# Kernel optimization log

Measured on AMD Instinct MI355X. Metric: run time of the kernel, lower is better.

The kernel has to match this reference:

```python
import jax, jax.numpy as jnp
import numpy as np

EPS = 1e-15
PROJ_EPS = 4e-3  # float32 boundary eps (geoopt convention)

def _artanh(x):
    return jnp.arctanh(jnp.clip(x, -1.0 + 1e-7, 1.0 - 1e-7))

def _norm(x, axis=-1):
    return jnp.maximum(jnp.sqrt(jnp.sum(x * x, axis=axis, keepdims=True)), EPS)

def expmap0(u, c):
    sc = jnp.sqrt(c)
    n = _norm(u)
    return jnp.tanh(sc * n) * u / (sc * n)

def project(x, c):
    n = _norm(x)
    maxn = (1.0 - PROJ_EPS) / jnp.sqrt(c)
    return jnp.where(n > maxn, x / n * maxn, x)

def mobius_pointwise_mul(w, x, c):
    sc = jnp.sqrt(c)
    wx = w * x
    xn = _norm(x)
    wxn = _norm(wx)
    return jnp.tanh(wxn / xn * _artanh(sc * xn)) * wx / (wxn * sc)

def mobius_add(x, y, c):
    x2 = jnp.sum(x * x, -1, keepdims=True)
    y2 = jnp.sum(y * y, -1, keepdims=True)
    xy = jnp.sum(x * y, -1, keepdims=True)
    num = (1.0 + 2.0 * c * xy + c * y2) * x + (1.0 - c * x2) * y
    den = 1.0 + 2.0 * c * xy + (c ** 2) * x2 * y2
    return num / jnp.maximum(den, EPS)

def logmap0(y, c):
    sc = jnp.sqrt(c)
    n = _norm(y)
    return _artanh(sc * n) * y / (sc * n)

def weighted_midpoint_batched(mix, c):
    # mix: (B, D, L); feature axis = 1 (torch call: dim=0 per sample), reduce over L.
    lam = 2.0 / jnp.maximum(1.0 - c * jnp.sum(mix * mix, axis=1, keepdims=True), EPS)  # (B,1,L)
    nom = jnp.sum(lam * mix, axis=2)          # (B, D)
    den = jnp.sum(lam - 1.0, axis=2)          # (B, 1)
    den = jnp.where(den >= 0, jnp.maximum(den, 1e-10), jnp.minimum(den, -1e-10))
    tm = nom / den                            # (B, D) "two_mean"
    # mobius_scalar_mul(0.5, tm)
    sc = jnp.sqrt(c)
    n = _norm(tm)
    return jnp.tanh(0.5 * _artanh(sc * n)) * tm / (sc * n)

def setup_inputs() -> dict:
    key = jax.random.key(0)
    ks = jax.random.split(key, 7)
    B, O, L, D = 64, 1, 1024, 1024
    return {
        "query": jax.random.normal(ks[0], (B, O, D), jnp.float32),
        "context": jax.random.normal(ks[1], (B, L, D), jnp.float32),
        "delta_t": jax.random.uniform(ks[2], (B, 1, L), jnp.float32),
        "c": jnp.ones((1,), jnp.float32),
        "W_in": jax.random.normal(ks[3], (D, D), jnp.float32) / np.float32(np.sqrt(D)),
        "W_out": jax.random.normal(ks[4], (D, 2 * D), jnp.float32) / np.float32(np.sqrt(2 * D)),
        "ae": jax.random.normal(ks[5], (B, 1, 1), jnp.float32) * 0.1,
        "ab": jax.random.normal(ks[6], (B, 1, 1), jnp.float32) * 0.1,
    }

def reference(query, context, delta_t, c, W_in, W_out, ae, ab):
    # linear_in (attention_type='general'): no bias
    q = jnp.einsum('bod,ed->boe', query, W_in)                     # (B,O,D)
    scores = jnp.einsum('bod,bld->bol', q, context)                # (B,O,L)
    aw = jax.nn.softmax(scores, axis=-1)
    aw = project(expmap0(aw, c), c)                                # hyperbolic attn weights
    ctx_t = jnp.transpose(context, (0, 2, 1))                      # (B,D,L)
    mix = project(mobius_pointwise_mul(aw, ctx_t, c), c)           # (B,D,L)
    bt = jnp.exp(-ab * delta_t)                                    # (B,1,L)
    bt = project(expmap0(bt, c), c)
    tmp = project(mobius_pointwise_mul(ae, mix, c), c)
    tmp = project(mobius_pointwise_mul(tmp, bt, c), c)
    term2 = jax.nn.relu(tmp)
    mix = project(mobius_add(mix, term2, c), c)
    fin = weighted_midpoint_batched(mix, c)[:, None, :]            # (B,1,D)
    mixl = logmap0(fin, c)
    combined = jnp.concatenate([mixl, q], axis=-1)                 # (B,1,2D)
    out = jnp.tanh(jnp.einsum('boe,de->bod', combined, W_out))     # (B,1,D)
    return (out, aw)
```

## Files before the change

### kernel.cpp

```cpp
#include <hip/hip_runtime.h>
#include <math.h>

#define BB 64
#define LL 1024
#define DD 1024

typedef __attribute__((ext_vector_type(4))) _Float16 half4;

__device__ __forceinline__ float artanh_c(float x){
  x = fminf(fmaxf(x, -1.f + 1e-7f), 1.f - 1e-7f);
  return 0.5f * __logf((1.f + x) / (1.f - x));
}

__device__ __forceinline__ float wave_sum(float v){
  #pragma unroll
  for(int o = 32; o > 0; o >>= 1) v += __shfl_down(v, o, 64);
  return v;
}

__device__ __forceinline__ float block_sum(float v, float* red){
  v = wave_sum(v);
  int wid = threadIdx.x >> 6, lane = threadIdx.x & 63;
  __syncthreads();
  if(lane == 0) red[wid] = v;
  __syncthreads();
  if(wid == 0){
    float t = lane < 16 ? red[lane] : 0.f;
    #pragma unroll
    for(int o = 8; o > 0; o >>= 1) t += __shfl_down(t, o, 64);
    if(lane == 0) red[0] = t;
  }
  __syncthreads();
  return red[0];
}

__device__ __forceinline__ float block_max(float v, float* red){
  #pragma unroll
  for(int o = 32; o > 0; o >>= 1) v = fmaxf(v, __shfl_down(v, o, 64));
  int wid = threadIdx.x >> 6, lane = threadIdx.x & 63;
  __syncthreads();
  if(lane == 0) red[wid] = v;
  __syncthreads();
  if(wid == 0){
    float t = lane < 16 ? red[lane] : -INFINITY;
    #pragma unroll
    for(int o = 8; o > 0; o >>= 1) t = fmaxf(t, __shfl_down(t, o, 64));
    if(lane == 0) red[0] = t;
  }
  __syncthreads();
  return red[0];
}

__global__ void k_qproj(const float* __restrict__ query, const float* __restrict__ Win,
                        float* __restrict__ q){
  int wave = threadIdx.x >> 6, lane = threadIdx.x & 63;
  int e = blockIdx.x * 4 + wave;
  int b0 = blockIdx.y * 16;
  const float4* Wr = (const float4*)(Win + (size_t)e * DD);
  float4 w[4];
  #pragma unroll
  for(int j = 0; j < 4; j++) w[j] = Wr[j * 64 + lane];
  for(int bb = 0; bb < 16; bb++){
    int b = b0 + bb;
    const float4* qr = (const float4*)(query + (size_t)b * DD);
    float acc = 0.f;
    #pragma unroll
    for(int j = 0; j < 4; j++){
      float4 v = qr[j * 64 + lane];
      acc += w[j].x * v.x + w[j].y * v.y + w[j].z * v.z + w[j].w * v.w;
    }
    acc = wave_sum(acc);
    if(lane == 0) q[b * DD + e] = acc;
  }
}

__global__ void k_scores(const float* __restrict__ qv, const float* __restrict__ ctx,
                         float* __restrict__ scores, _Float16* __restrict__ ctx16){
  int b = blockIdx.y;
  int wave = threadIdx.x >> 6, lane = threadIdx.x & 63;
  int l = blockIdx.x * 4 + wave;
  __shared__ float4 qs4[DD / 4];
  if(threadIdx.x < 256) qs4[threadIdx.x] = ((const float4*)(qv + (size_t)b * DD))[threadIdx.x];
  __syncthreads();
  const float4* cr = (const float4*)(ctx + ((size_t)b * LL + l) * DD);
  half4* c16 = (half4*)(ctx16 + ((size_t)b * LL + l) * DD);
  float acc = 0.f;
  #pragma unroll
  for(int it = 0; it < 4; it++){
    int idx = it * 64 + lane;
    float4 v = cr[idx];
    float4 qq = qs4[idx];
    acc += qq.x * v.x + qq.y * v.y + qq.z * v.z + qq.w * v.w;
    half4 h;
    h.x = (_Float16)v.x; h.y = (_Float16)v.y; h.z = (_Float16)v.z; h.w = (_Float16)v.w;
    c16[idx] = h;
  }
  acc = wave_sum(acc);
  if(lane == 0) scores[b * LL + l] = acc;
}

__global__ void k_softmax_tr(const float* __restrict__ scores, const float* __restrict__ dt,
                             const float* __restrict__ ab, const float* __restrict__ cp,
                             float* __restrict__ awt, float* __restrict__ aw_out,
                             float* __restrict__ btt, float* __restrict__ btn){
  __shared__ float red[16];
  int b = blockIdx.x, tid = threadIdx.x;
  float c = cp[0], sc = sqrtf(c), maxn = (1.f - 4e-3f) / sc;
  float s = scores[b * LL + tid];
  float m = block_max(s, red);
  float e = __expf(s - m);
  float Z = block_sum(e, red);
  float aw = e / Z;
  float S = block_sum(aw * aw, red);
  float n = fmaxf(sqrtf(S), 1e-15f);
  float tau = tanhf(sc * n) / (sc * n);
  float n1 = fmaxf(tau * sqrtf(S), 1e-15f);
  float s1 = n1 > maxn ? maxn / n1 : 1.f;
  float awf = tau * s1 * aw;
  awt[b * LL + tid] = awf;
  aw_out[b * LL + tid] = awf;
  float btv = __expf(-ab[b] * dt[b * LL + tid]);
  float S2 = block_sum(btv * btv, red);
  float n2 = fmaxf(sqrtf(S2), 1e-15f);
  float tau2 = tanhf(sc * n2) / (sc * n2);
  float nb = fmaxf(tau2 * sqrtf(S2), 1e-15f);
  float s2 = nb > maxn ? maxn / nb : 1.f;
  float btf = tau2 * s2 * btv;
  btt[b * LL + tid] = btf;
  if(tid == 0) btn[b] = fmaxf(tau2 * s2 * sqrtf(S2), 1e-15f);
}

__global__ __launch_bounds__(256) void k_stats(const _Float16* __restrict__ ctx16,
                        const float* __restrict__ awt,
                        const float* __restrict__ btt, float* __restrict__ stats){
  int tid = threadIdx.x;
  int b = blockIdx.x;
  int l0 = blockIdx.y * 128;
  __shared__ float ws_[128], bs_[128];
  if(tid < 128){ ws_[tid] = awt[b * LL + l0 + tid]; bs_[tid] = btt[b * LL + l0 + tid]; }
  __syncthreads();
  const half4* cpx = (const half4*)(ctx16 + ((size_t)b * LL + l0) * DD) + tid;
  float r2[4] = {0,0,0,0}, p2[4] = {0,0,0,0};
  float s3p[4] = {0,0,0,0}, s3m[4] = {0,0,0,0};
  float s5p[4] = {0,0,0,0}, s5m[4] = {0,0,0,0};
  #pragma unroll 4
  for(int i = 0; i < 128; i++){
    half4 hv = cpx[(size_t)i * (DD / 4)];
    float w = ws_[i], bt = bs_[i];
    float rr[4] = {(float)hv.x, (float)hv.y, (float)hv.z, (float)hv.w};
    #pragma unroll
    for(int c = 0; c < 4; c++){
      float r = rr[c];
      float p = w * r;
      r2[c] = fmaf(r, r, r2[c]);
      p2[c] = fmaf(p, p, p2[c]);
      float pb = p * bt;
      float pb2 = pb * pb;
      float p2bt = (p * p) * bt;
      if(r > 0.f){ s3p[c] += pb2; s5p[c] += p2bt; } else { s3m[c] += pb2; s5m[c] += p2bt; }
    }
  }
  int d = tid * 4;
  float* base = stats + (size_t)b * 6 * DD + d;
  #pragma unroll
  for(int c = 0; c < 4; c++){
    atomicAdd(base + 0 * DD + c, r2[c]);
    atomicAdd(base + 1 * DD + c, p2[c]);
    atomicAdd(base + 2 * DD + c, s3p[c]);
    atomicAdd(base + 3 * DD + c, s3m[c]);
    atomicAdd(base + 4 * DD + c, s5p[c]);
    atomicAdd(base + 5 * DD + c, s5m[c]);
  }
}

__global__ void k_finish(const float* __restrict__ stats, const float* __restrict__ ae,
                         const float* __restrict__ btn, const float* __restrict__ cp,
                         float* __restrict__ rowsc){
  int row = blockIdx.x * 256 + threadIdx.x;
  int b = row >> 10;
  int d = row & (DD - 1);
  float c = cp[0], sc = sqrtf(c), maxn = (1.f - 4e-3f) / sc;
  const float* st = stats + (size_t)b * 6 * DD + d;
  float r2 = st[0], p2 = st[DD], s3p = st[2 * DD], s3m = st[3 * DD], s5p = st[4 * DD], s5m = st[5 * DD];
  float sp2 = sqrtf(p2);
  float xn  = fmaxf(sqrtf(r2), 1e-15f);
  float wxn = fmaxf(sp2, 1e-15f);
  float at1 = artanh_c(sc * xn);
  float alpha = tanhf(wxn / xn * at1) / (wxn * sc);
  float n1 = fmaxf(alpha * sp2, 1e-15f);
  float beta = alpha * (n1 > maxn ? maxn / n1 : 1.f);
  float aeb = ae[b];
  float mixn_raw = beta * sp2;
  float xn2  = fmaxf(mixn_raw, 1e-15f);
  float wxn2 = fmaxf(fabsf(aeb) * mixn_raw, 1e-15f);
  float at2 = artanh_c(sc * xn2);
  float coef_t = tanhf(wxn2 / xn2 * at2) * aeb * beta / (wxn2 * sc);
  float n2 = fmaxf(fabsf(coef_t) * sp2, 1e-15f);
  float g = coef_t * (n2 > maxn ? maxn / n2 : 1.f);
  float s3 = s3p + s3m;
  float sq3 = sqrtf(s3);
  float xn3 = btn[b];
  float wxn3 = fmaxf(fabsf(g) * sq3, 1e-15f);
  float at3 = artanh_c(sc * xn3);
  float coef2 = tanhf(wxn3 / xn3 * at3) * g / (wxn3 * sc);
  float n3 = fmaxf(fabsf(coef2) * sq3, 1e-15f);
  float k = coef2 * (n3 > maxn ? maxn / n3 : 1.f);
  bool kp = k > 0.f;
  float ssel  = kp ? s3p : s3m;
  float s5sel = kp ? s5p : s5m;
  float y2 = k * k * ssel;
  float xy = beta * k * s5sel;
  float x2 = beta * beta * p2;
  float A  = 1.f + 2.f * c * xy + c * y2;
  float Bc = 1.f - c * x2;
  float den = 1.f + 2.f * c * xy + c * c * x2 * y2;
  den = fmaxf(den, 1e-15f);
  float U0 = A * beta / den;
  float V0 = Bc * k / den;
  float nf2 = U0 * U0 * p2 + 2.f * U0 * V0 * s5sel + V0 * V0 * ssel;
  float nf = fmaxf(sqrtf(nf2), 1e-15f);
  float s4 = nf > maxn ? maxn / nf : 1.f;
  float U = U0 * s4, V = V0 * s4;
  float4* out4 = (float4*)(rowsc + (size_t)row * 4);
  *out4 = make_float4(U, kp ? V : 0.f, kp ? 0.f : V, 0.f);
}

__global__ __launch_bounds__(256) void k_mixagg(const _Float16* __restrict__ ctx16,
                         const float* __restrict__ awt, const float* __restrict__ btt,
                         const float* __restrict__ rowsc, const float* __restrict__ cp,
                         float* __restrict__ lam_out, float* __restrict__ nom){
  __shared__ float aw_s[32], bt_s[32], lam_s[32];
  int b = blockIdx.y;
  int l0 = blockIdx.x * 32;
  int tid = threadIdx.x, wave = tid >> 6, lane = tid & 63;
  float c = cp[0];
  if(tid < 32){ aw_s[tid] = awt[b * LL + l0 + tid]; bt_s[tid] = btt[b * LL + l0 + tid]; }
  float U1[4][4], Vp1[4][4], Vm1[4][4];
  const float4* rp = (const float4*)rowsc + (size_t)b * DD;
  #pragma unroll
  for(int it = 0; it < 4; it++){
    int d4 = it * 64 + lane;
    #pragma unroll
    for(int j = 0; j < 4; j++){
      float4 t = rp[d4 * 4 + j];
      U1[it][j] = t.x; Vp1[it][j] = t.y; Vm1[it][j] = t.z;
    }
  }
  float U2[4], Vp2[4], Vm2[4];
  #pragma unroll
  for(int j = 0; j < 4; j++){
    float4 t = rp[tid * 4 + j];
    U2[j] = t.x; Vp2[j] = t.y; Vm2[j] = t.z;
  }
  __syncthreads();
  const half4* cb = (const half4*)(ctx16 + (size_t)b * LL * DD);
  #pragma unroll
  for(int rr = 0; rr < 8; rr++){
    int r = wave + rr * 4;
    int l = l0 + r;
    float w = aw_s[r], bt = bt_s[r];
    float acc = 0.f;
    #pragma unroll
    for(int it = 0; it < 4; it++){
      half4 hv = cb[(size_t)l * (DD / 4) + it * 64 + lane];
      float rx[4] = {(float)hv.x, (float)hv.y, (float)hv.z, (float)hv.w};
      #pragma unroll
      for(int j = 0; j < 4; j++){
        float rc = rx[j];
        float p = w * rc;
        float t = rc > 0.f ? Vp1[it][j] : Vm1[it][j];
        float mv = p * (U1[it][j] + bt * t);
        acc = fmaf(mv, mv, acc);
      }
    }
    acc = wave_sum(acc);
    if(lane == 0){
      float lv = 2.f / fmaxf(1.f - c * acc, 1e-15f);
      lam_s[r] = lv;
      lam_out[b * LL + l] = lv;
    }
  }
  __syncthreads();
  float acc2[4] = {0, 0, 0, 0};
  #pragma unroll 4
  for(int r = 0; r < 32; r++){
    float w = aw_s[r], bt = bt_s[r], lv = lam_s[r];
    half4 hv = cb[(size_t)(l0 + r) * (DD / 4) + tid];
    float rx[4] = {(float)hv.x, (float)hv.y, (float)hv.z, (float)hv.w};
    #pragma unroll
    for(int j = 0; j < 4; j++){
      float rc = rx[j];
      float p = w * rc;
      float t = rc > 0.f ? Vp2[j] : Vm2[j];
      float mv = p * (U2[j] + bt * t);
      acc2[j] = fmaf(lv, mv, acc2[j]);
    }
  }
  #pragma unroll
  for(int j = 0; j < 4; j++) atomicAdd(nom + (size_t)b * DD + tid * 4 + j, acc2[j]);
}

__global__ void k_mid(const float* __restrict__ nom, const float* __restrict__ lam,
                      const float* __restrict__ qv, const float* __restrict__ cp,
                      float* __restrict__ comb){
  __shared__ float red[16];
  int b = blockIdx.x, tid = threadIdx.x;
  float c = cp[0], sc = sqrtf(c);
  float lv = lam[b * LL + tid];
  float dsum = block_sum(lv - 1.f, red);
  float den = dsum >= 0.f ? fmaxf(dsum, 1e-10f) : fminf(dsum, -1e-10f);
  float tm = nom[b * DD + tid] / den;
  float S = block_sum(tm * tm, red);
  float n = fmaxf(sqrtf(S), 1e-15f);
  float at = artanh_c(sc * n);
  float mu = tanhf(0.5f * at) / (sc * n);
  float n2 = fmaxf(mu * sqrtf(S), 1e-15f);
  float nu = artanh_c(sc * n2) / (sc * n2);
  comb[b * 2 * DD + tid] = nu * mu * tm;
  comb[b * 2 * DD + DD + tid] = qv[b * DD + tid];
}

__global__ void k_out(const float* __restrict__ comb, const float* __restrict__ Wout,
                      float* __restrict__ outp){
  int wave = threadIdx.x >> 6, lane = threadIdx.x & 63;
  int d = blockIdx.x * 4 + wave;
  int b0 = blockIdx.y * 16;
  const float4* Wr = (const float4*)(Wout + (size_t)d * 2 * DD);
  float4 w[8];
  #pragma unroll
  for(int j = 0; j < 8; j++) w[j] = Wr[j * 64 + lane];
  for(int bb = 0; bb < 16; bb++){
    int b = b0 + bb;
    const float4* cb = (const float4*)(comb + (size_t)b * 2 * DD);
    float acc = 0.f;
    #pragma unroll
    for(int j = 0; j < 8; j++){
      float4 v = cb[j * 64 + lane];
      acc += w[j].x * v.x + w[j].y * v.y + w[j].z * v.z + w[j].w * v.w;
    }
    acc = wave_sum(acc);
    if(lane == 0) outp[b * DD + d] = tanhf(acc);
  }
}

extern "C" void kernel_launch(void* const* d_in, const int* in_sizes, int n_in,
                              void* d_out, int out_size, void* d_ws, size_t ws_size,
                              hipStream_t stream) {
  const float* query = (const float*)d_in[0];
  const float* ctx   = (const float*)d_in[1];
  const float* dt    = (const float*)d_in[2];
  const float* cp    = (const float*)d_in[3];
  const float* Win   = (const float*)d_in[4];
  const float* Wout  = (const float*)d_in[5];
  const float* ae    = (const float*)d_in[6];
  const float* ab    = (const float*)d_in[7];
  float* out = (float*)d_out;
  float* ws  = (float*)d_ws;

  float* q_      = ws;
  float* awt_    = ws + 65536;
  float* btt_    = ws + 131072;
  float* btn_    = ws + 196608;
  float* scores_ = ws + 196672;
  float* stats_  = ws + 262208;
  float* nom_    = ws + 655424;
  float* rowsc_  = ws + 720960;
  _Float16* ctx16_ = (_Float16*)(ws + 983104);
  float* lam_  = scores_;
  float* comb_ = stats_;

  hipMemsetAsync(stats_, 0, (size_t)(393216 + 65536) * sizeof(float), stream);

  k_qproj     <<<dim3(256, 4),  256,  0, stream>>>(query, Win, q_);
  k_scores    <<<dim3(256, BB), 256,  0, stream>>>(q_, ctx, scores_, ctx16_);
  k_softmax_tr<<<BB,            1024, 0, stream>>>(scores_, dt, ab, cp, awt_, out + BB * DD, btt_, btn_);
  k_stats     <<<dim3(BB, 8),   256,  0, stream>>>(ctx16_, awt_, btt_, stats_);
  k_finish    <<<256,           256,  0, stream>>>(stats_, ae, btn_, cp, rowsc_);
  k_mixagg    <<<dim3(32, BB),  256,  0, stream>>>(ctx16_, awt_, btt_, rowsc_, cp, lam_, nom_);
  k_mid       <<<BB,            1024, 0, stream>>>(nom_, lam_, q_, cp, comb_);
  k_out       <<<dim3(256, 4),  256,  0, stream>>>(comb_, Wout, out);
}
```

Measured before the change: 598.9 us.

## Replace atomics with partial-sum buffers, vectorize reductions, widen fp16 loads

Replaces the atomicAdd accumulation in the stats and mixagg kernels with per-block partial buffers that the finish and mid kernels reduce, which removes the memset and atomic contention. It also moves the stats inner loop to half8 loads with precomputed w², w²·bt and w²·bt² factors, and adds nontemporal loads of the fp32 context. The softmax and mid kernels shrink to 256 threads with float4 elements and a simpler 4-wave block reduction. The partial buffers cost extra workspace and extra read traffic in the reducing kernels.

```diff
diff --git a/kernel.cpp b/kernel.cpp
--- a/kernel.cpp
+++ b/kernel.cpp
@@ -6,6 +6,8 @@
 #define DD 1024
 
 typedef __attribute__((ext_vector_type(4))) _Float16 half4;
+typedef __attribute__((ext_vector_type(8))) _Float16 half8;
+typedef __attribute__((ext_vector_type(4))) float f32x4;
 
 __device__ __forceinline__ float artanh_c(float x){
   x = fminf(fmaxf(x, -1.f + 1e-7f), 1.f - 1e-7f);
@@ -18,37 +20,25 @@
   return v;
 }
 
-__device__ __forceinline__ float block_sum(float v, float* red){
+__device__ __forceinline__ float block_sum4(float v, float* red){
   v = wave_sum(v);
   int wid = threadIdx.x >> 6, lane = threadIdx.x & 63;
-  __syncthreads();
   if(lane == 0) red[wid] = v;
   __syncthreads();
-  if(wid == 0){
-    float t = lane < 16 ? red[lane] : 0.f;
-    #pragma unroll
-    for(int o = 8; o > 0; o >>= 1) t += __shfl_down(t, o, 64);
-    if(lane == 0) red[0] = t;
-  }
-  __syncthreads();
-  return red[0];
-}
-
-__device__ __forceinline__ float block_max(float v, float* red){
+  float t = red[0] + red[1] + red[2] + red[3];
+  __syncthreads();
+  return t;
+}
+
+__device__ __forceinline__ float block_max4(float v, float* red){
   #pragma unroll
   for(int o = 32; o > 0; o >>= 1) v = fmaxf(v, __shfl_down(v, o, 64));
   int wid = threadIdx.x >> 6, lane = threadIdx.x & 63;
-  __syncthreads();
   if(lane == 0) red[wid] = v;
   __syncthreads();
-  if(wid == 0){
-    float t = lane < 16 ? red[lane] : -INFINITY;
-    #pragma unroll
-    for(int o = 8; o > 0; o >>= 1) t = fmaxf(t, __shfl_down(t, o, 64));
-    if(lane == 0) red[0] = t;
-  }
-  __syncthreads();
-  return red[0];
+  float t = fmaxf(fmaxf(red[0], red[1]), fmaxf(red[2], red[3]));
+  __syncthreads();
+  return t;
 }
 
 __global__ void k_qproj(const float* __restrict__ query, const float* __restrict__ Win,
@@ -80,15 +70,15 @@
   int wave = threadIdx.x >> 6, lane = threadIdx.x & 63;
   int l = blockIdx.x * 4 + wave;
   __shared__ float4 qs4[DD / 4];
-  if(threadIdx.x < 256) qs4[threadIdx.x] = ((const float4*)(qv + (size_t)b * DD))[threadIdx.x];
-  __syncthreads();
-  const float4* cr = (const float4*)(ctx + ((size_t)b * LL + l) * DD);
+  qs4[threadIdx.x] = ((const float4*)(qv + (size_t)b * DD))[threadIdx.x];
+  __syncthreads();
+  const f32x4* cr = (const f32x4*)(ctx + ((size_t)b * LL + l) * DD);
   half4* c16 = (half4*)(ctx16 + ((size_t)b * LL + l) * DD);
   float acc = 0.f;
   #pragma unroll
   for(int it = 0; it < 4; it++){
     int idx = it * 64 + lane;
-    float4 v = cr[idx];
+    f32x4 v = __builtin_nontemporal_load(&cr[idx]);
     float4 qq = qs4[idx];
     acc += qq.x * v.x + qq.y * v.y + qq.z * v.z + qq.w * v.w;
     half4 h;
@@ -103,85 +93,104 @@
                              const float* __restrict__ ab, const float* __restrict__ cp,
                              float* __restrict__ awt, float* __restrict__ aw_out,
                              float* __restrict__ btt, float* __restrict__ btn){
-  __shared__ float red[16];
+  __shared__ float red[4];
   int b = blockIdx.x, tid = threadIdx.x;
   float c = cp[0], sc = sqrtf(c), maxn = (1.f - 4e-3f) / sc;
-  float s = scores[b * LL + tid];
-  float m = block_max(s, red);
-  float e = __expf(s - m);
-  float Z = block_sum(e, red);
-  float aw = e / Z;
-  float S = block_sum(aw * aw, red);
+  float4 s = ((const float4*)(scores + (size_t)b * LL))[tid];
+  float m = block_max4(fmaxf(fmaxf(s.x, s.y), fmaxf(s.z, s.w)), red);
+  float4 e;
+  e.x = __expf(s.x - m); e.y = __expf(s.y - m); e.z = __expf(s.z - m); e.w = __expf(s.w - m);
+  float Z = block_sum4(e.x + e.y + e.z + e.w, red);
+  float inv = 1.f / Z;
+  float4 aw;
+  aw.x = e.x * inv; aw.y = e.y * inv; aw.z = e.z * inv; aw.w = e.w * inv;
+  float S = block_sum4(aw.x * aw.x + aw.y * aw.y + aw.z * aw.z + aw.w * aw.w, red);
   float n = fmaxf(sqrtf(S), 1e-15f);
   float tau = tanhf(sc * n) / (sc * n);
   float n1 = fmaxf(tau * sqrtf(S), 1e-15f);
   float s1 = n1 > maxn ? maxn / n1 : 1.f;
-  float awf = tau * s1 * aw;
-  awt[b * LL + tid] = awf;
-  aw_out[b * LL + tid] = awf;
-  float btv = __expf(-ab[b] * dt[b * LL + tid]);
-  float S2 = block_sum(btv * btv, red);
+  float f = tau * s1;
+  float4 awf;
+  awf.x = f * aw.x; awf.y = f * aw.y; awf.z = f * aw.z; awf.w = f * aw.w;
+  ((float4*)(awt + (size_t)b * LL))[tid] = awf;
+  ((float4*)(aw_out + (size_t)b * LL))[tid] = awf;
+  float4 d4 = ((const float4*)(dt + (size_t)b * LL))[tid];
+  float abv = ab[b];
+  float4 bv;
+  bv.x = __expf(-abv * d4.x); bv.y = __expf(-abv * d4.y);
+  bv.z = __expf(-abv * d4.z); bv.w = __expf(-abv * d4.w);
+  float S2 = block_sum4(bv.x * bv.x + bv.y * bv.y + bv.z * bv.z + bv.w * bv.w, red);
   float n2 = fmaxf(sqrtf(S2), 1e-15f);
   float tau2 = tanhf(sc * n2) / (sc * n2);
   float nb = fmaxf(tau2 * sqrtf(S2), 1e-15f);
-  float s2 = nb > maxn ? maxn / nb : 1.f;
-  float btf = tau2 * s2 * btv;
-  btt[b * LL + tid] = btf;
-  if(tid == 0) btn[b] = fmaxf(tau2 * s2 * sqrtf(S2), 1e-15f);
+  float s2f = nb > maxn ? maxn / nb : 1.f;
+  float f2 = tau2 * s2f;
+  float4 btf;
+  btf.x = f2 * bv.x; btf.y = f2 * bv.y; btf.z = f2 * bv.z; btf.w = f2 * bv.w;
+  ((float4*)(btt + (size_t)b * LL))[tid] = btf;
+  if(tid == 0) btn[b] = fmaxf(f2 * sqrtf(S2), 1e-15f);
 }
 
 __global__ __launch_bounds__(256) void k_stats(const _Float16* __restrict__ ctx16,
                         const float* __restrict__ awt,
-                        const float* __restrict__ btt, float* __restrict__ stats){
+                        const float* __restrict__ btt, float* __restrict__ stats16){
   int tid = threadIdx.x;
   int b = blockIdx.x;
+  int oct = tid & 127, h = tid >> 7;
   int l0 = blockIdx.y * 128;
-  __shared__ float ws_[128], bs_[128];
-  if(tid < 128){ ws_[tid] = awt[b * LL + l0 + tid]; bs_[tid] = btt[b * LL + l0 + tid]; }
-  __syncthreads();
-  const half4* cpx = (const half4*)(ctx16 + ((size_t)b * LL + l0) * DD) + tid;
-  float r2[4] = {0,0,0,0}, p2[4] = {0,0,0,0};
-  float s3p[4] = {0,0,0,0}, s3m[4] = {0,0,0,0};
-  float s5p[4] = {0,0,0,0}, s5m[4] = {0,0,0,0};
-  #pragma unroll 4
-  for(int i = 0; i < 128; i++){
-    half4 hv = cpx[(size_t)i * (DD / 4)];
-    float w = ws_[i], bt = bs_[i];
-    float rr[4] = {(float)hv.x, (float)hv.y, (float)hv.z, (float)hv.w};
-    #pragma unroll
-    for(int c = 0; c < 4; c++){
-      float r = rr[c];
-      float p = w * r;
-      r2[c] = fmaf(r, r, r2[c]);
-      p2[c] = fmaf(p, p, p2[c]);
-      float pb = p * bt;
-      float pb2 = pb * pb;
-      float p2bt = (p * p) * bt;
-      if(r > 0.f){ s3p[c] += pb2; s5p[c] += p2bt; } else { s3m[c] += pb2; s5m[c] += p2bt; }
-    }
-  }
-  int d = tid * 4;
-  float* base = stats + (size_t)b * 6 * DD + d;
-  #pragma unroll
-  for(int c = 0; c < 4; c++){
-    atomicAdd(base + 0 * DD + c, r2[c]);
-    atomicAdd(base + 1 * DD + c, p2[c]);
-    atomicAdd(base + 2 * DD + c, s3p[c]);
-    atomicAdd(base + 3 * DD + c, s3m[c]);
-    atomicAdd(base + 4 * DD + c, s5p[c]);
-    atomicAdd(base + 5 * DD + c, s5m[c]);
-  }
-}
-
-__global__ void k_finish(const float* __restrict__ stats, const float* __restrict__ ae,
+  __shared__ float w2_[128], w2b_[128], w2b2_[128];
+  if(tid < 128){
+    float w = awt[b * LL + l0 + tid], bt = btt[b * LL + l0 + tid];
+    float w2 = w * w;
+    w2_[tid] = w2; w2b_[tid] = w2 * bt; w2b2_[tid] = w2 * bt * bt;
+  }
+  __syncthreads();
+  const half8* cpx = (const half8*)(ctx16 + ((size_t)b * LL + l0 + h * 64) * DD) + oct;
+  float r2[8] = {0,0,0,0,0,0,0,0}, p2[8] = {0,0,0,0,0,0,0,0};
+  float s3p[8] = {0,0,0,0,0,0,0,0}, s3m[8] = {0,0,0,0,0,0,0,0};
+  float s5p[8] = {0,0,0,0,0,0,0,0}, s5m[8] = {0,0,0,0,0,0,0,0};
+  #pragma unroll 8
+  for(int i = 0; i < 64; i++){
+    half8 hv = cpx[(size_t)i * 128];
+    int li = h * 64 + i;
+    float w2 = w2_[li], w2b = w2b_[li], w2b2 = w2b2_[li];
+    #pragma unroll
+    for(int j = 0; j < 8; j++){
+      float r = (float)hv[j];
+      float rsq = r * r;
+      float rp2 = r > 0.f ? rsq : 0.f;
+      float rn2 = rsq - rp2;
+      r2[j] += rsq;
+      p2[j] = fmaf(w2, rsq, p2[j]);
+      s3p[j] = fmaf(w2b2, rp2, s3p[j]);
+      s3m[j] = fmaf(w2b2, rn2, s3m[j]);
+      s5p[j] = fmaf(w2b, rp2, s5p[j]);
+      s5m[j] = fmaf(w2b, rn2, s5m[j]);
+    }
+  }
+  float* sl = stats16 + (((size_t)b * 16 + (size_t)blockIdx.y * 2 + h) * 6) * DD + oct * 8;
+  #define ST_(sidx, arr) { float4* o = (float4*)(sl + (sidx) * DD); \
+    o[0] = make_float4(arr[0], arr[1], arr[2], arr[3]); \
+    o[1] = make_float4(arr[4], arr[5], arr[6], arr[7]); }
+  ST_(0, r2) ST_(1, p2) ST_(2, s3p) ST_(3, s3m) ST_(4, s5p) ST_(5, s5m)
+  #undef ST_
+}
+
+__global__ void k_finish(const float* __restrict__ stats16, const float* __restrict__ ae,
                          const float* __restrict__ btn, const float* __restrict__ cp,
                          float* __restrict__ rowsc){
   int row = blockIdx.x * 256 + threadIdx.x;
   int b = row >> 10;
   int d = row & (DD - 1);
   float c = cp[0], sc = sqrtf(c), maxn = (1.f - 4e-3f) / sc;
-  const float* st = stats + (size_t)b * 6 * DD + d;
-  float r2 = st[0], p2 = st[DD], s3p = st[2 * DD], s3m = st[3 * DD], s5p = st[4 * DD], s5m = st[5 * DD];
+  const float* st = stats16 + (size_t)b * 16 * 6 * DD + d;
+  float r2 = 0.f, p2 = 0.f, s3p = 0.f, s3m = 0.f, s5p = 0.f, s5m = 0.f;
+  #pragma unroll
+  for(int g = 0; g < 16; g++){
+    const float* sg = st + (size_t)g * 6 * DD;
+    r2 += sg[0]; p2 += sg[DD]; s3p += sg[2 * DD];
+    s3m += sg[3 * DD]; s5p += sg[4 * DD]; s5m += sg[5 * DD];
+  }
   float sp2 = sqrtf(p2);
   float xn  = fmaxf(sqrtf(r2), 1e-15f);
   float wxn = fmaxf(sp2, 1e-15f);
@@ -228,21 +237,21 @@
 __global__ __launch_bounds__(256) void k_mixagg(const _Float16* __restrict__ ctx16,
                          const float* __restrict__ awt, const float* __restrict__ btt,
                          const float* __restrict__ rowsc, const float* __restrict__ cp,
-                         float* __restrict__ lam_out, float* __restrict__ nom){
+                         float* __restrict__ lam_out, float* __restrict__ nom32){
   __shared__ float aw_s[32], bt_s[32], lam_s[32];
   int b = blockIdx.y;
   int l0 = blockIdx.x * 32;
   int tid = threadIdx.x, wave = tid >> 6, lane = tid & 63;
   float c = cp[0];
   if(tid < 32){ aw_s[tid] = awt[b * LL + l0 + tid]; bt_s[tid] = btt[b * LL + l0 + tid]; }
-  float U1[4][4], Vp1[4][4], Vm1[4][4];
+  float U1[2][8], Vp1[2][8], Vm1[2][8];
   const float4* rp = (const float4*)rowsc + (size_t)b * DD;
   #pragma unroll
-  for(int it = 0; it < 4; it++){
-    int d4 = it * 64 + lane;
-    #pragma unroll
-    for(int j = 0; j < 4; j++){
-      float4 t = rp[d4 * 4 + j];
+  for(int it = 0; it < 2; it++){
+    int o = it * 64 + lane;
+    #pragma unroll
+    for(int j = 0; j < 8; j++){
+      float4 t = rp[o * 8 + j];
       U1[it][j] = t.x; Vp1[it][j] = t.y; Vm1[it][j] = t.z;
     }
   }
@@ -253,7 +262,7 @@
     U2[j] = t.x; Vp2[j] = t.y; Vm2[j] = t.z;
   }
   __syncthreads();
-  const half4* cb = (const half4*)(ctx16 + (size_t)b * LL * DD);
+  const half8* cb8 = (const half8*)(ctx16 + (size_t)b * LL * DD);
   #pragma unroll
   for(int rr = 0; rr < 8; rr++){
     int r = wave + rr * 4;
@@ -261,63 +270,71 @@
     float w = aw_s[r], bt = bt_s[r];
     float acc = 0.f;
     #pragma unroll
-    for(int it = 0; it < 4; it++){
-      half4 hv = cb[(size_t)l * (DD / 4) + it * 64 + lane];
-      float rx[4] = {(float)hv.x, (float)hv.y, (float)hv.z, (float)hv.w};
+    for(int it = 0; it < 2; it++){
+      half8 hv = cb8[(size_t)l * 128 + it * 64 + lane];
       #pragma unroll
-      for(int j = 0; j < 4; j++){
-        float rc = rx[j];
-        float p = w * rc;
+      for(int j = 0; j < 8; j++){
+        float rc = (float)hv[j];
         float t = rc > 0.f ? Vp1[it][j] : Vm1[it][j];
-        float mv = p * (U1[it][j] + bt * t);
-        acc = fmaf(mv, mv, acc);
+        float uv = fmaf(bt, t, U1[it][j]);
+        float mvs = rc * uv;
+        acc = fmaf(mvs, mvs, acc);
       }
     }
     acc = wave_sum(acc);
     if(lane == 0){
-      float lv = 2.f / fmaxf(1.f - c * acc, 1e-15f);
+      float lv = 2.f / fmaxf(1.f - c * (w * w) * acc, 1e-15f);
       lam_s[r] = lv;
       lam_out[b * LL + l] = lv;
     }
   }
   __syncthreads();
   float acc2[4] = {0, 0, 0, 0};
+  const half4* cb4 = (const half4*)(ctx16 + (size_t)b * LL * DD);
   #pragma unroll 4
   for(int r = 0; r < 32; r++){
-    float w = aw_s[r], bt = bt_s[r], lv = lam_s[r];
-    half4 hv = cb[(size_t)(l0 + r) * (DD / 4) + tid];
+    float bt = bt_s[r];
+    float lw = lam_s[r] * aw_s[r];
+    half4 hv = cb4[(size_t)(l0 + r) * 256 + tid];
     float rx[4] = {(float)hv.x, (float)hv.y, (float)hv.z, (float)hv.w};
     #pragma unroll
     for(int j = 0; j < 4; j++){
       float rc = rx[j];
-      float p = w * rc;
       float t = rc > 0.f ? Vp2[j] : Vm2[j];
-      float mv = p * (U2[j] + bt * t);
-      acc2[j] = fmaf(lv, mv, acc2[j]);
-    }
-  }
-  #pragma unroll
-  for(int j = 0; j < 4; j++) atomicAdd(nom + (size_t)b * DD + tid * 4 + j, acc2[j]);
-}
-
-__global__ void k_mid(const float* __restrict__ nom, const float* __restrict__ lam,
+      float mv = rc * fmaf(bt, t, U2[j]);
+      acc2[j] = fmaf(lw, mv, acc2[j]);
+    }
+  }
+  ((float4*)(nom32 + ((size_t)b * 32 + blockIdx.x) * DD))[tid] =
+      make_float4(acc2[0], acc2[1], acc2[2], acc2[3]);
+}
+
+__global__ void k_mid(const float* __restrict__ nom32, const float* __restrict__ lam,
                       const float* __restrict__ qv, const float* __restrict__ cp,
                       float* __restrict__ comb){
-  __shared__ float red[16];
+  __shared__ float red[4];
   int b = blockIdx.x, tid = threadIdx.x;
   float c = cp[0], sc = sqrtf(c);
-  float lv = lam[b * LL + tid];
-  float dsum = block_sum(lv - 1.f, red);
+  float4 lv = ((const float4*)(lam + (size_t)b * LL))[tid];
+  float dsum = block_sum4(lv.x + lv.y + lv.z + lv.w - 4.f, red);
   float den = dsum >= 0.f ? fmaxf(dsum, 1e-10f) : fminf(dsum, -1e-10f);
-  float tm = nom[b * DD + tid] / den;
-  float S = block_sum(tm * tm, red);
+  float nx = 0.f, ny = 0.f, nz = 0.f, nw = 0.f;
+  #pragma unroll
+  for(int k = 0; k < 32; k++){
+    float4 t = ((const float4*)(nom32 + ((size_t)b * 32 + k) * DD))[tid];
+    nx += t.x; ny += t.y; nz += t.z; nw += t.w;
+  }
+  float tx = nx / den, ty = ny / den, tz = nz / den, tw = nw / den;
+  float S = block_sum4(tx * tx + ty * ty + tz * tz + tw * tw, red);
   float n = fmaxf(sqrtf(S), 1e-15f);
   float at = artanh_c(sc * n);
   float mu = tanhf(0.5f * at) / (sc * n);
   float n2 = fmaxf(mu * sqrtf(S), 1e-15f);
   float nu = artanh_c(sc * n2) / (sc * n2);
-  comb[b * 2 * DD + tid] = nu * mu * tm;
-  comb[b * 2 * DD + DD + tid] = qv[b * DD + tid];
+  float f = nu * mu;
+  float4 q4 = ((const float4*)(qv + (size_t)b * DD))[tid];
+  ((float4*)(comb + (size_t)b * 2 * DD))[tid] = make_float4(f * tx, f * ty, f * tz, f * tw);
+  ((float4*)(comb + (size_t)b * 2 * DD + DD))[tid] = q4;
 }
 
 __global__ void k_out(const float* __restrict__ comb, const float* __restrict__ Wout,
@@ -357,26 +374,24 @@
   float* out = (float*)d_out;
   float* ws  = (float*)d_ws;
 
-  float* q_      = ws;
-  float* awt_    = ws + 65536;
-  float* btt_    = ws + 131072;
-  float* btn_    = ws + 196608;
-  float* scores_ = ws + 196672;
-  float* stats_  = ws + 262208;
-  float* nom_    = ws + 655424;
-  float* rowsc_  = ws + 720960;
-  _Float16* ctx16_ = (_Float16*)(ws + 983104);
-  float* lam_  = scores_;
-  float* comb_ = stats_;
-
-  hipMemsetAsync(stats_, 0, (size_t)(393216 + 65536) * sizeof(float), stream);
-
-  k_qproj     <<<dim3(256, 4),  256,  0, stream>>>(query, Win, q_);
-  k_scores    <<<dim3(256, BB), 256,  0, stream>>>(q_, ctx, scores_, ctx16_);
-  k_softmax_tr<<<BB,            1024, 0, stream>>>(scores_, dt, ab, cp, awt_, out + BB * DD, btt_, btn_);
-  k_stats     <<<dim3(BB, 8),   256,  0, stream>>>(ctx16_, awt_, btt_, stats_);
-  k_finish    <<<256,           256,  0, stream>>>(stats_, ae, btn_, cp, rowsc_);
-  k_mixagg    <<<dim3(32, BB),  256,  0, stream>>>(ctx16_, awt_, btt_, rowsc_, cp, lam_, nom_);
-  k_mid       <<<BB,            1024, 0, stream>>>(nom_, lam_, q_, cp, comb_);
-  k_out       <<<dim3(256, 4),  256,  0, stream>>>(comb_, Wout, out);
-}
+  float* q_       = ws;
+  float* awt_     = ws + 65536;
+  float* btt_     = ws + 131072;
+  float* btn_     = ws + 196608;
+  float* scores_  = ws + 196736;
+  float* rowsc_   = ws + 262272;
+  float* comb_    = ws + 524416;
+  float* stats16_ = ws + 655488;
+  float* nom32_   = ws + 6946944;
+  _Float16* ctx16_ = (_Float16*)(ws + 9044096);
+  float* lam_ = scores_;
+
+  k_qproj     <<<dim3(256, 4),  256, 0, stream>>>(query, Win, q_);
+  k_scores    <<<dim3(256, BB), 256, 0, stream>>>(q_, ctx, scores_, ctx16_);
+  k_softmax_tr<<<BB,            256, 0, stream>>>(scores_, dt, ab, cp, awt_, out + BB * DD, btt_, btn_);
+  k_stats     <<<dim3(BB, 8),   256, 0, stream>>>(ctx16_, awt_, btt_, stats16_);
+  k_finish    <<<256,           256, 0, stream>>>(stats16_, ae, btn_, cp, rowsc_);
+  k_mixagg    <<<dim3(32, BB),  256, 0, stream>>>(ctx16_, awt_, btt_, rowsc_, cp, lam_, nom32_);
+  k_mid       <<<BB,            256, 0, stream>>>(nom32_, lam_, q_, cp, comb_);
+  k_out       <<<dim3(256, 4),  256, 0, stream>>>(comb_, Wout, out);
+}
```

Result: faster. 498.3 us (-16.8%).
